# Performance work log

Measured on AMD Instinct MI355X. Metric: run time of the kernel, lower is better.

## Reference

```python
import jax, jax.numpy as jnp
import numpy as np

B, S, D, H = 4, 2048, 1024, 16
HD = D // H  # head_size = 64


def setup_inputs() -> dict:
    key = jax.random.key(0)
    ks = jax.random.split(key, 9)
    sc = 0.02
    x = jax.random.normal(ks[0], (B, S, D), dtype=jnp.float32)
    Wq = jax.random.normal(ks[1], (H, D, HD), dtype=jnp.float32) * sc
    Wk = jax.random.normal(ks[2], (H, D, HD), dtype=jnp.float32) * sc
    Wv = jax.random.normal(ks[3], (H, D, HD), dtype=jnp.float32) * sc
    bq = jax.random.normal(ks[4], (H, HD), dtype=jnp.float32) * sc
    bk = jax.random.normal(ks[5], (H, HD), dtype=jnp.float32) * sc
    bv = jax.random.normal(ks[6], (H, HD), dtype=jnp.float32) * sc
    Wp = jax.random.normal(ks[7], (D, D), dtype=jnp.float32) * sc
    bp = jax.random.normal(ks[8], (D,), dtype=jnp.float32) * sc
    return {"x": x, "Wq": Wq, "bq": bq, "Wk": Wk, "bk": bk,
            "Wv": Wv, "bv": bv, "Wp": Wp, "bp": bp}


def reference(x, Wq, bq, Wk, bk, Wv, bv, Wp, bp):
    # Per-head Linear q/k/v, batched over heads with einsum (equivalent math
    # to the original Python loop over SingleHeadAttention modules).
    q = jnp.einsum('bsd,hde->bhse', x, Wq) + bq[None, :, None, :]
    k = jnp.einsum('bsd,hde->bhse', x, Wk) + bk[None, :, None, :]
    v = jnp.einsum('bsd,hde->bhse', x, Wv) + bv[None, :, None, :]
    att = jnp.einsum('bhqe,bhke->bhqk', q, k) / jnp.sqrt(jnp.asarray(HD, q.dtype))
    causal = jnp.tril(jnp.ones((S, S), dtype=bool))  # [S,S]
    att = jnp.where(causal[None, None], att, jnp.finfo(att.dtype).min)
    w = jax.nn.softmax(att, axis=-1)
    o = jnp.einsum('bhqk,bhke->bhqe', w, v)           # [B,H,S,HD]
    o = o.transpose(0, 2, 1, 3).reshape(B, S, D)      # concat heads on last dim
    # output projection; dropout is identity in eval (p=0.0)
    return jnp.einsum('bsd,de->bse', o, Wp) + bp
```

## Files before the change

kernel.cpp:

```cpp
#include <hip/hip_runtime.h>
#include <hip/hip_bf16.h>

typedef __attribute__((ext_vector_type(8)))  short bf16x8;
typedef __attribute__((ext_vector_type(4)))  float f32x4;
typedef __attribute__((ext_vector_type(16))) float f32x16;
typedef __attribute__((ext_vector_type(2)))  int   i32x2;

#define NH  16
#define HD  64
#define SEQ 2048
#define DM  1024
#define NB  4

#define QSCALE 0.18033688011112042f

#define MFMA(a,b,c)   __builtin_amdgcn_mfma_f32_16x16x32_bf16((a),(b),(c),0,0,0)
#define MFMA32(a,b,c) __builtin_amdgcn_mfma_f32_32x32x16_bf16((a),(b),(c),0,0,0)

static __device__ __forceinline__ void gload_lds16(const void* g, void* l) {
    __builtin_amdgcn_global_load_lds(
        (const __attribute__((address_space(1))) void*)g,
        (__attribute__((address_space(3))) void*)l, 16, 0, 0);
}

__global__ __launch_bounds__(256)
void prep(const float* __restrict__ x,  const float* __restrict__ Wq,
          const float* __restrict__ Wk, const float* __restrict__ Wv,
          const float* __restrict__ Wp,
          __hip_bfloat16* __restrict__ xb,  __hip_bfloat16* __restrict__ wqt,
          __hip_bfloat16* __restrict__ wkt, __hip_bfloat16* __restrict__ wvt,
          __hip_bfloat16* __restrict__ wpt) {
    const long XE = (long)NB * SEQ * DM;
    const long CAST_T = XE / 8;
    long gid = (long)blockIdx.x * 256 + threadIdx.x;
    if (gid < CAST_T) {
        long i = gid * 8;
        float4 a = *reinterpret_cast<const float4*>(x + i);
        float4 b = *reinterpret_cast<const float4*>(x + i + 4);
        ushort4 o1, o2;
        o1.x = __bfloat16_as_ushort(__float2bfloat16(a.x));
        o1.y = __bfloat16_as_ushort(__float2bfloat16(a.y));
        o1.z = __bfloat16_as_ushort(__float2bfloat16(a.z));
        o1.w = __bfloat16_as_ushort(__float2bfloat16(a.w));
        o2.x = __bfloat16_as_ushort(__float2bfloat16(b.x));
        o2.y = __bfloat16_as_ushort(__float2bfloat16(b.y));
        o2.z = __bfloat16_as_ushort(__float2bfloat16(b.z));
        o2.w = __bfloat16_as_ushort(__float2bfloat16(b.w));
        *reinterpret_cast<ushort4*>(xb + i)     = o1;
        *reinterpret_cast<ushort4*>(xb + i + 4) = o2;
        return;
    }
    long r = gid - CAST_T;
    const long WQK = 1 << 20;
    if (r < 3 * WQK) {
        int z = (int)(r >> 20);
        long idx = r & (WQK - 1);
        const float* src = (z == 0) ? Wq : (z == 1) ? Wk : Wv;
        __hip_bfloat16* dst = (z == 0) ? wqt : (z == 1) ? wkt : wvt;
        int c  = (int)(idx & 63);
        long t2 = idx >> 6;
        int rr = (int)(t2 & 1023);
        int mm = (int)(t2 >> 10);
        dst[((long)mm * HD + c) * DM + rr] = __float2bfloat16(src[idx]);
    } else {
        long idx = r - 3 * WQK;
        int c  = (int)(idx & 1023);
        int rr = (int)(idx >> 10);
        wpt[(long)c * DM + rr] = __float2bfloat16(Wp[idx]);
    }
}

__global__ __launch_bounds__(256)
void qkv_gemm(const __hip_bfloat16* __restrict__ A,
              const __hip_bfloat16* __restrict__ BT,
              const float* __restrict__ b0,
              const float* __restrict__ b1,
              const float* __restrict__ b2,
              __hip_bfloat16* __restrict__ Qo,
              __hip_bfloat16* __restrict__ Ko,
              __hip_bfloat16* __restrict__ Vto) {
    __shared__ __align__(16) char lds[2][32768];
    int tid = threadIdx.x;
    int w = tid >> 6, l = tid & 63;
    int lr = l & 15, lg = l >> 4;
    int wr = w >> 1, wc = w & 1;
    int mtile = blockIdx.x, ntile = blockIdx.y;
    const int AR0 = mtile * 128, BR0 = ntile * 128;

    const int rsub = w * 8 + (l >> 3);
    const int sg0 = l & 7;
    auto stage = [&](const __hip_bfloat16* g, int grow0, int kc, char* lbase) {
#pragma unroll
        for (int i = 0; i < 4; ++i) {
            int row = i * 32 + rsub;
            gload_lds16(g + (long)(grow0 + row) * DM + kc + ((sg0 ^ (row & 7)) << 3),
                        lbase + i * 4096 + w * 1024);
        }
    };

    int aoff[4][2], boff[4][2];
#pragma unroll
    for (int m = 0; m < 4; ++m) {
        int ra = wr * 64 + m * 16 + lr;
        int rb = wc * 64 + m * 16 + lr;
#pragma unroll
        for (int kh = 0; kh < 2; ++kh) {
            aoff[m][kh] = ra * 128 + (((kh * 4 + lg) ^ (ra & 7)) << 4);
            boff[m][kh] = 16384 + rb * 128 + (((kh * 4 + lg) ^ (rb & 7)) << 4);
        }
    }

    f32x4 acc[4][4] = {};

    stage(A,  AR0, 0, lds[0]);
    stage(BT, BR0, 0, lds[0] + 16384);
    __syncthreads();

    int cur = 0;
    for (int kt = 0; kt < 16; ++kt) {
        if (kt < 15) {
            int kc = (kt + 1) * 64;
            stage(A,  AR0, kc, lds[cur ^ 1]);
            stage(BT, BR0, kc, lds[cur ^ 1] + 16384);
        }
        bf16x8 bf[4][2];
#pragma unroll
        for (int n = 0; n < 4; ++n) {
            bf[n][0] = *(const bf16x8*)(lds[cur] + boff[n][0]);
            bf[n][1] = *(const bf16x8*)(lds[cur] + boff[n][1]);
        }
#pragma unroll
        for (int m = 0; m < 4; ++m) {
            bf16x8 a0 = *(const bf16x8*)(lds[cur] + aoff[m][0]);
            bf16x8 a1 = *(const bf16x8*)(lds[cur] + aoff[m][1]);
#pragma unroll
            for (int n = 0; n < 4; ++n) {
                acc[m][n] = MFMA(a0, bf[n][0], acc[m][n]);
                acc[m][n] = MFMA(a1, bf[n][1], acc[m][n]);
            }
        }
        __syncthreads();
        cur ^= 1;
    }

    int z = ntile >> 3;
    const float* bias = (z == 0) ? b0 : (z == 1) ? b1 : b2;
    int colbase = (ntile & 7) * 128 + wc * 64;
#pragma unroll
    for (int n = 0; n < 4; ++n) {
        int hc = colbase + n * 16 + lr;
        int h = hc >> 6, e = hc & 63;
        float bb = bias[hc];
#pragma unroll
        for (int m = 0; m < 4; ++m) {
            int row0 = mtile * 128 + wr * 64 + m * 16 + lg * 4;
            int b = row0 >> 11, s0 = row0 & 2047;
            if (z == 0) {
#pragma unroll
                for (int r = 0; r < 4; ++r)
                    Qo[(((long)b * NH + h) * SEQ + s0 + r) * HD + e] =
                        __float2bfloat16((acc[m][n][r] + bb) * QSCALE);
            } else if (z == 1) {
#pragma unroll
                for (int r = 0; r < 4; ++r)
                    Ko[(((long)b * NH + h) * SEQ + s0 + r) * HD + e] =
                        __float2bfloat16(acc[m][n][r] + bb);
            } else {
                ushort4 s4;
                s4.x = __bfloat16_as_ushort(__float2bfloat16(acc[m][n][0] + bb));
                s4.y = __bfloat16_as_ushort(__float2bfloat16(acc[m][n][1] + bb));
                s4.z = __bfloat16_as_ushort(__float2bfloat16(acc[m][n][2] + bb));
                s4.w = __bfloat16_as_ushort(__float2bfloat16(acc[m][n][3] + bb));
                *reinterpret_cast<ushort4*>(
                    Vto + ((long)(b * NH + h) * HD + e) * SEQ + s0) = s4;
            }
        }
    }
}

__global__ __launch_bounds__(256)
void out_gemm(const __hip_bfloat16* __restrict__ A,
              const __hip_bfloat16* __restrict__ BT,
              const float* __restrict__ b0,
              float* __restrict__ Fo) {
    __shared__ __align__(16) char smem[2][16384];
    int tid = threadIdx.x;
    int w = tid >> 6, l = tid & 63;
    int wr = w >> 1, wc = w & 1;
    int lr = l & 15, lg = l >> 4;
    int mtile = blockIdx.x, ntile = blockIdx.y;

    const __hip_bfloat16* Ab = A  + (long)mtile * 128 * DM;
    const __hip_bfloat16* Bb = BT + (long)ntile * 128 * DM;

    const int srow0 = tid >> 2;
    const int srow1 = 64 + srow0;
    const int g0 = (tid & 3) ^ ((srow0 >> 1) & 3);

    int aoff[4], boff[4];
#pragma unroll
    for (int m = 0; m < 4; ++m) {
        int ra = wr * 64 + m * 16 + lr;
        aoff[m] = ra * 64 + ((lg ^ ((ra >> 1) & 3)) * 16);
        int rb = wc * 64 + m * 16 + lr;
        boff[m] = 8192 + rb * 64 + ((lg ^ ((rb >> 1) & 3)) * 16);
    }

    f32x4 acc[4][4] = {};

    {
        char* base = smem[0] + w * 1024;
        gload_lds16(Ab + (long)srow0 * DM + g0 * 8, base);
        gload_lds16(Ab + (long)srow1 * DM + g0 * 8, base + 4096);
        gload_lds16(Bb + (long)srow0 * DM + g0 * 8, base + 8192);
        gload_lds16(Bb + (long)srow1 * DM + g0 * 8, base + 12288);
    }
    __syncthreads();

    int cur = 0;
    for (int kt = 0; kt < 32; ++kt) {
        if (kt != 31) {
            int k0 = (kt + 1) * 32;
            char* base = smem[cur ^ 1] + w * 1024;
            gload_lds16(Ab + (long)srow0 * DM + k0 + g0 * 8, base);
            gload_lds16(Ab + (long)srow1 * DM + k0 + g0 * 8, base + 4096);
            gload_lds16(Bb + (long)srow0 * DM + k0 + g0 * 8, base + 8192);
            gload_lds16(Bb + (long)srow1 * DM + k0 + g0 * 8, base + 12288);
        }
        bf16x8 af[4], bf[4];
#pragma unroll
        for (int m = 0; m < 4; ++m)
            af[m] = *reinterpret_cast<const bf16x8*>(smem[cur] + aoff[m]);
#pragma unroll
        for (int n = 0; n < 4; ++n)
            bf[n] = *reinterpret_cast<const bf16x8*>(smem[cur] + boff[n]);
#pragma unroll
        for (int m = 0; m < 4; ++m)
#pragma unroll
            for (int n = 0; n < 4; ++n)
                acc[m][n] = MFMA(af[m], bf[n], acc[m][n]);
        __syncthreads();
        cur ^= 1;
    }

#pragma unroll
    for (int n = 0; n < 4; ++n) {
        int col = ntile * 128 + wc * 64 + n * 16 + lr;
        float bb = b0[col];
#pragma unroll
        for (int m = 0; m < 4; ++m) {
            long row0 = mtile * 128 + wr * 64 + m * 16 + lg * 4;
#pragma unroll
            for (int r = 0; r < 4; ++r)
                Fo[(row0 + r) * DM + col] = acc[m][n][r] + bb;
        }
    }
}

static __device__ __forceinline__ unsigned pkbf(float a, float b) {
    __hip_bfloat162 h = __float22bfloat162_rn(float2{a, b});
    union { __hip_bfloat162 h2; unsigned u; } u_; u_.h2 = h;
    return u_.u;
}
static __device__ __forceinline__ bf16x8 make_pb(unsigned w0, unsigned w1,
                                                 unsigned w2, unsigned w3) {
    union { unsigned u[4]; bf16x8 v; } u_;
    u_.u[0] = w0; u_.u[1] = w1; u_.u[2] = w2; u_.u[3] = w3;
    return u_.v;
}
static __device__ __forceinline__ i32x2 pl32swap(unsigned a, unsigned b) {
    return __builtin_amdgcn_permlane32_swap((int)a, (int)b, false, false);
}
static __device__ __forceinline__ float xsum32(float x) {
    i32x2 r = pl32swap(__float_as_uint(x), __float_as_uint(x));
    return __uint_as_float((unsigned)r[0]) + __uint_as_float((unsigned)r[1]);
}

template<bool MASKED>
static __device__ __forceinline__ void attn_tile(
    const bf16x8* kf, const bf16x8* qf, const bf16x8* vf,
    int lo5, int hi,
    f32x16& o0, f32x16& o1, float& lsum) {
    f32x16 st = {};
    __builtin_amdgcn_s_setprio(1);
#pragma unroll
    for (int kd = 0; kd < 4; ++kd) st = MFMA32(kf[kd], qf[kd], st);
    __builtin_amdgcn_s_setprio(0);
    if (MASKED) {
#pragma unroll
        for (int r = 0; r < 16; ++r) {
            int kvloc = (r & 3) + 8 * (r >> 2) + 4 * hi;
            st[r] = (kvloc > lo5) ? -INFINITY : st[r];
        }
    }
    float p[16];
#pragma unroll
    for (int r = 0; r < 16; ++r) p[r] = __builtin_amdgcn_exp2f(st[r]);
    float s0 = (p[0] + p[1]) + (p[2] + p[3]);
    float s1 = (p[4] + p[5]) + (p[6] + p[7]);
    float s2 = (p[8] + p[9]) + (p[10] + p[11]);
    float s3 = (p[12] + p[13]) + (p[14] + p[15]);
    lsum += (s0 + s1) + (s2 + s3);

    unsigned pk0 = pkbf(p[0],  p[1]),  pk1 = pkbf(p[2],  p[3]);
    unsigned pk2 = pkbf(p[4],  p[5]),  pk3 = pkbf(p[6],  p[7]);
    unsigned pk4 = pkbf(p[8],  p[9]),  pk5 = pkbf(p[10], p[11]);
    unsigned pk6 = pkbf(p[12], p[13]), pk7 = pkbf(p[14], p[15]);
    i32x2 s02 = pl32swap(pk0, pk2);
    i32x2 s13 = pl32swap(pk1, pk3);
    i32x2 s46 = pl32swap(pk4, pk6);
    i32x2 s57 = pl32swap(pk5, pk7);
    bf16x8 pb0 = make_pb((unsigned)s02[0], (unsigned)s13[0],
                         (unsigned)s02[1], (unsigned)s13[1]);
    bf16x8 pb1 = make_pb((unsigned)s46[0], (unsigned)s57[0],
                         (unsigned)s46[1], (unsigned)s57[1]);

    __builtin_amdgcn_s_setprio(1);
    o0 = MFMA32(vf[0], pb0, o0);
    o1 = MFMA32(vf[1], pb0, o1);
    o0 = MFMA32(vf[2], pb1, o0);
    o1 = MFMA32(vf[3], pb1, o1);
    __builtin_amdgcn_s_setprio(0);
}

__global__ __launch_bounds__(256)
void flash_attn(const __hip_bfloat16* __restrict__ Q,
                const __hip_bfloat16* __restrict__ K,
                const __hip_bfloat16* __restrict__ Vt,
                __hip_bfloat16* __restrict__ O) {
    __shared__ __align__(16) char kv[2][8192];
    int bh = blockIdx.x;
    int w  = threadIdx.x >> 6, l = threadIdx.x & 63;
    int lo5 = l & 31, hi = l >> 5;
    int y  = blockIdx.y;
    int pr = y * 4 + w;
    int jA = pr, jB = 63 - pr;
    int q0A = jA * 32, q0B = jB * 32;
    const int TMAX = 63 - 4 * y;

    const __hip_bfloat16* Qh = Q  + (long)bh * SEQ * HD;
    const __hip_bfloat16* Kh = K  + (long)bh * SEQ * HD;
    const __hip_bfloat16* Vh = Vt + (long)bh * HD * SEQ;

    bf16x8 qfA[4], qfB[4];
#pragma unroll
    for (int kd = 0; kd < 4; ++kd) {
        qfA[kd] = *reinterpret_cast<const bf16x8*>(
            Qh + (long)(q0A + lo5) * HD + kd * 16 + hi * 8);
        qfB[kd] = *reinterpret_cast<const bf16x8*>(
            Qh + (long)(q0B + lo5) * HD + kd * 16 + hi * 8);
    }

    int srow = w * 8 + (l >> 3);
    int kslot = (l & 7) ^ (srow & 7);
    const __hip_bfloat16* ksrc = Kh + (long)srow * HD + kslot * 8;
    int vlog = (l & 7) ^ (srow & 7);
    int vrow = srow + ((vlog >> 2) << 5);
    const __hip_bfloat16* vsrc = Vh + (long)vrow * SEQ + (vlog & 3) * 8;

    int ka[4], va[4];
#pragma unroll
    for (int kd = 0; kd < 4; ++kd)
        ka[kd] = lo5 * 128 + (((kd * 2 + hi) ^ (lo5 & 7)) << 4);
    va[0] = 4096 + lo5 * 128 + (((0 + hi) ^ (lo5 & 7)) << 4);
    va[1] = 4096 + lo5 * 128 + (((4 + hi) ^ (lo5 & 7)) << 4);
    va[2] = 4096 + lo5 * 128 + (((2 + hi) ^ (lo5 & 7)) << 4);
    va[3] = 4096 + lo5 * 128 + (((6 + hi) ^ (lo5 & 7)) << 4);

    f32x16 oA0 = {}, oA1 = {}, oB0 = {}, oB1 = {};
    float lsA = 0.f, lsB = 0.f;

    gload_lds16(ksrc, kv[0] + w * 1024);
    gload_lds16(vsrc, kv[0] + 4096 + w * 1024);
    __syncthreads();

    int buf = 0;
    for (int t = 0; t <= TMAX; ++t) {
        if (t < TMAX) {
            gload_lds16(ksrc + (long)(t + 1) * 32 * HD, kv[buf ^ 1] + w * 1024);
            gload_lds16(vsrc + (t + 1) * 32,            kv[buf ^ 1] + 4096 + w * 1024);
        }
        const char* cb = kv[buf];
        bf16x8 kf[4], vf[4];
#pragma unroll
        for (int kd = 0; kd < 4; ++kd)
            kf[kd] = *reinterpret_cast<const bf16x8*>(cb + ka[kd]);
#pragma unroll
        for (int j = 0; j < 4; ++j)
            vf[j] = *reinterpret_cast<const bf16x8*>(cb + va[j]);

        if (t < jA) {
            attn_tile<false>(kf, qfB, vf, lo5, hi, oB0, oB1, lsB);
            attn_tile<false>(kf, qfA, vf, lo5, hi, oA0, oA1, lsA);
        } else if (t == jA) {
            attn_tile<true >(kf, qfA, vf, lo5, hi, oA0, oA1, lsA);
            attn_tile<false>(kf, qfB, vf, lo5, hi, oB0, oB1, lsB);
        } else if (t < jB) {
            attn_tile<false>(kf, qfB, vf, lo5, hi, oB0, oB1, lsB);
        } else if (t == jB) {
            attn_tile<true >(kf, qfB, vf, lo5, hi, oB0, oB1, lsB);
        }
        __syncthreads();
        buf ^= 1;
    }

    int b = bh >> 4, h = bh & 15;
    float invA = 1.0f / xsum32(lsA);
    float invB = 1.0f / xsum32(lsB);
#pragma unroll
    for (int c = 0; c < 2; ++c) {
        int q0 = c ? q0B : q0A;
        const f32x16& o0 = c ? oB0 : oA0;
        const f32x16& o1 = c ? oB1 : oA1;
        float inv = c ? invB : invA;
        __hip_bfloat16* orow = O + ((long)b * SEQ + q0 + lo5) * DM + h * HD;
#pragma unroll
        for (int nd = 0; nd < 2; ++nd) {
#pragma unroll
            for (int rg = 0; rg < 4; ++rg) {
                ushort4 s4;
                float a0 = (nd ? o1[rg * 4 + 0] : o0[rg * 4 + 0]) * inv;
                float a1 = (nd ? o1[rg * 4 + 1] : o0[rg * 4 + 1]) * inv;
                float a2 = (nd ? o1[rg * 4 + 2] : o0[rg * 4 + 2]) * inv;
                float a3 = (nd ? o1[rg * 4 + 3] : o0[rg * 4 + 3]) * inv;
                s4.x = __bfloat16_as_ushort(__float2bfloat16(a0));
                s4.y = __bfloat16_as_ushort(__float2bfloat16(a1));
                s4.z = __bfloat16_as_ushort(__float2bfloat16(a2));
                s4.w = __bfloat16_as_ushort(__float2bfloat16(a3));
                *reinterpret_cast<ushort4*>(orow + nd * 32 + rg * 8 + hi * 4) = s4;
            }
        }
    }
}

extern "C" void kernel_launch(void* const* d_in, const int* in_sizes, int n_in,
                              void* d_out, int out_size, void* d_ws, size_t ws_size,
                              hipStream_t stream) {
    const float* x  = (const float*)d_in[0];
    const float* Wq = (const float*)d_in[1];
    const float* bq = (const float*)d_in[2];
    const float* Wk = (const float*)d_in[3];
    const float* bk = (const float*)d_in[4];
    const float* Wv = (const float*)d_in[5];
    const float* bv = (const float*)d_in[6];
    const float* Wp = (const float*)d_in[7];
    const float* bp = (const float*)d_in[8];
    float* out = (float*)d_out;

    char* ws = (char*)d_ws;
    const long XE = (long)NB * SEQ * DM;
    const long QKV_ELEMS = (long)NB * NH * SEQ * HD;
    __hip_bfloat16* xb   = (__hip_bfloat16*)ws; ws += XE * 2;
    __hip_bfloat16* Qws  = (__hip_bfloat16*)ws; ws += QKV_ELEMS * 2;
    __hip_bfloat16* Kws  = (__hip_bfloat16*)ws; ws += QKV_ELEMS * 2;
    __hip_bfloat16* Vtws = (__hip_bfloat16*)ws; ws += QKV_ELEMS * 2;
    __hip_bfloat16* Ows  = (__hip_bfloat16*)ws; ws += QKV_ELEMS * 2;
    __hip_bfloat16* wqt  = (__hip_bfloat16*)ws; ws += (long)NH * DM * HD * 2;
    __hip_bfloat16* wkt  = (__hip_bfloat16*)ws; ws += (long)NH * DM * HD * 2;
    __hip_bfloat16* wvt  = (__hip_bfloat16*)ws; ws += (long)NH * DM * HD * 2;
    __hip_bfloat16* wpt  = (__hip_bfloat16*)ws; ws += (long)DM * DM * 2;

    prep<<<20480, 256, 0, stream>>>(x, Wq, Wk, Wv, Wp, xb, wqt, wkt, wvt, wpt);

    qkv_gemm<<<dim3(64, 24), 256, 0, stream>>>(
        xb, wqt, bq, bk, bv, Qws, Kws, Vtws);

    flash_attn<<<dim3(64, 8), 256, 0, stream>>>(Qws, Kws, Vtws, Ows);

    out_gemm<<<dim3(64, 8), 256, 0, stream>>>(Ows, wpt, bp, out);
}
```

Baseline: 185.4 us.

## Use 256x256 tiles with 4-stage pipelined loads for QKV GEMM

The QKV projection GEMM moves from 128x128 tiles with 256 threads and double buffering to 256x256 tiles with 512 threads, a 4-buffer LDS ring with three tiles in flight, explicit vmcnt waits, s_setprio around the MFMA block, and an XCD-aware block swizzle. The out-projection GEMM switches to the 64-wide K-step, 8-way swizzled staging scheme the old QKV kernel used. The aim is more operand reuse per LDS byte, better hiding of global latency and better L2 locality. In exchange it needs 128KB of LDS per block and more accumulator registers, which limits occupancy, and the grid becomes 384 blocks.

```diff
diff --git a/kernel.cpp b/kernel.cpp
--- a/kernel.cpp
+++ b/kernel.cpp
@@ -70,90 +70,100 @@
     }
 }
 
-__global__ __launch_bounds__(256)
-void qkv_gemm(const __hip_bfloat16* __restrict__ A,
-              const __hip_bfloat16* __restrict__ BT,
-              const float* __restrict__ b0,
-              const float* __restrict__ b1,
-              const float* __restrict__ b2,
-              __hip_bfloat16* __restrict__ Qo,
-              __hip_bfloat16* __restrict__ Ko,
-              __hip_bfloat16* __restrict__ Vto) {
-    __shared__ __align__(16) char lds[2][32768];
+__global__ __launch_bounds__(512, 2)
+void qkv_gemm256(const __hip_bfloat16* __restrict__ A,
+                 const __hip_bfloat16* __restrict__ BT,
+                 const float* __restrict__ b0,
+                 const float* __restrict__ b1,
+                 const float* __restrict__ b2,
+                 __hip_bfloat16* __restrict__ Qo,
+                 __hip_bfloat16* __restrict__ Ko,
+                 __hip_bfloat16* __restrict__ Vto) {
+    __shared__ __align__(16) char lds[4][32768];
     int tid = threadIdx.x;
-    int w = tid >> 6, l = tid & 63;
+    int wid = tid >> 6, l = tid & 63;
     int lr = l & 15, lg = l >> 4;
-    int wr = w >> 1, wc = w & 1;
-    int mtile = blockIdx.x, ntile = blockIdx.y;
-    const int AR0 = mtile * 128, BR0 = ntile * 128;
-
-    const int rsub = w * 8 + (l >> 3);
-    const int sg0 = l & 7;
-    auto stage = [&](const __hip_bfloat16* g, int grow0, int kc, char* lbase) {
-#pragma unroll
-        for (int i = 0; i < 4; ++i) {
-            int row = i * 32 + rsub;
-            gload_lds16(g + (long)(grow0 + row) * DM + kc + ((sg0 ^ (row & 7)) << 3),
-                        lbase + i * 4096 + w * 1024);
-        }
-    };
-
-    int aoff[4][2], boff[4][2];
-#pragma unroll
-    for (int m = 0; m < 4; ++m) {
-        int ra = wr * 64 + m * 16 + lr;
-        int rb = wc * 64 + m * 16 + lr;
-#pragma unroll
-        for (int kh = 0; kh < 2; ++kh) {
-            aoff[m][kh] = ra * 128 + (((kh * 4 + lg) ^ (ra & 7)) << 4);
-            boff[m][kh] = 16384 + rb * 128 + (((kh * 4 + lg) ^ (rb & 7)) << 4);
-        }
-    }
-
-    f32x4 acc[4][4] = {};
-
-    stage(A,  AR0, 0, lds[0]);
-    stage(BT, BR0, 0, lds[0] + 16384);
-    __syncthreads();
-
-    int cur = 0;
-    for (int kt = 0; kt < 16; ++kt) {
-        if (kt < 15) {
-            int kc = (kt + 1) * 64;
-            stage(A,  AR0, kc, lds[cur ^ 1]);
-            stage(BT, BR0, kc, lds[cur ^ 1] + 16384);
-        }
-        bf16x8 bf[4][2];
-#pragma unroll
-        for (int n = 0; n < 4; ++n) {
-            bf[n][0] = *(const bf16x8*)(lds[cur] + boff[n][0]);
-            bf[n][1] = *(const bf16x8*)(lds[cur] + boff[n][1]);
-        }
-#pragma unroll
-        for (int m = 0; m < 4; ++m) {
-            bf16x8 a0 = *(const bf16x8*)(lds[cur] + aoff[m][0]);
-            bf16x8 a1 = *(const bf16x8*)(lds[cur] + aoff[m][1]);
-#pragma unroll
-            for (int n = 0; n < 4; ++n) {
-                acc[m][n] = MFMA(a0, bf[n][0], acc[m][n]);
-                acc[m][n] = MFMA(a1, bf[n][1], acc[m][n]);
-            }
-        }
-        __syncthreads();
-        cur ^= 1;
-    }
-
-    int z = ntile >> 3;
+    int wr = wid >> 2, wc = wid & 3;
+
+    int lin = blockIdx.y * 32 + blockIdx.x;
+    int swz = (lin & 7) * 48 + (lin >> 3);
+    int mtile = swz & 31, ntile = swz >> 5;
+    const int  AR0 = mtile * 256;
+    const long BR0 = (long)ntile * 256;
+
+    const int srow = tid >> 2;
+    const int sg   = tid & 3;
+
+    int aoff[8], boff[4];
+#pragma unroll
+    for (int m = 0; m < 8; ++m) {
+        int R = wr * 128 + m * 16 + lr;
+        aoff[m] = R * 64 + (((lg) ^ (R & 3)) << 4);
+    }
+#pragma unroll
+    for (int n = 0; n < 4; ++n) {
+        int R = wc * 64 + n * 16 + lr;
+        boff[n] = 16384 + R * 64 + (((lg) ^ (R & 3)) << 4);
+    }
+
+    f32x4 acc[8][4] = {};
+
+#define STAGE_T(T, BUFI)                                                      \
+    {                                                                         \
+        int kc_ = (T) * 32;                                                   \
+        char* base_ = lds[BUFI];                                              \
+        _Pragma("unroll")                                                     \
+        for (int i_ = 0; i_ < 2; ++i_) {                                      \
+            int row_ = i_ * 128 + srow;                                       \
+            int g_ = sg ^ (row_ & 3);                                         \
+            gload_lds16(A + (long)(AR0 + row_) * DM + kc_ + g_ * 8,           \
+                        base_ + i_ * 8192 + wid * 1024);                      \
+            gload_lds16(BT + (BR0 + row_) * DM + kc_ + g_ * 8,                \
+                        base_ + 16384 + i_ * 8192 + wid * 1024);              \
+        }                                                                     \
+    }
+
+    STAGE_T(0, 0) STAGE_T(1, 1) STAGE_T(2, 2)
+
+#pragma unroll 4
+    for (int t = 0; t < 32; ++t) {
+        const int bufi = t & 3;
+        if (t < 29) STAGE_T(t + 3, (t + 3) & 3)
+        if (t < 29)      { asm volatile("s_waitcnt vmcnt(12)" ::: "memory"); }
+        else if (t == 29){ asm volatile("s_waitcnt vmcnt(8)"  ::: "memory"); }
+        else if (t == 30){ asm volatile("s_waitcnt vmcnt(4)"  ::: "memory"); }
+        else             { asm volatile("s_waitcnt vmcnt(0)"  ::: "memory"); }
+        __builtin_amdgcn_s_barrier();
+        __builtin_amdgcn_sched_barrier(0);
+        const char* cb = lds[bufi];
+        bf16x8 bfr[4];
+#pragma unroll
+        for (int n = 0; n < 4; ++n)
+            bfr[n] = *reinterpret_cast<const bf16x8*>(cb + boff[n]);
+        __builtin_amdgcn_s_setprio(1);
+#pragma unroll
+        for (int m = 0; m < 8; ++m) {
+            bf16x8 a = *reinterpret_cast<const bf16x8*>(cb + aoff[m]);
+#pragma unroll
+            for (int n = 0; n < 4; ++n)
+                acc[m][n] = MFMA(a, bfr[n], acc[m][n]);
+        }
+        __builtin_amdgcn_s_setprio(0);
+        __builtin_amdgcn_s_barrier();
+    }
+#undef STAGE_T
+
+    int z = ntile >> 2;
     const float* bias = (z == 0) ? b0 : (z == 1) ? b1 : b2;
-    int colbase = (ntile & 7) * 128 + wc * 64;
+    int cb0 = (ntile & 3) * 256 + wc * 64;
 #pragma unroll
     for (int n = 0; n < 4; ++n) {
-        int hc = colbase + n * 16 + lr;
+        int hc = cb0 + n * 16 + lr;
         int h = hc >> 6, e = hc & 63;
         float bb = bias[hc];
 #pragma unroll
-        for (int m = 0; m < 4; ++m) {
-            int row0 = mtile * 128 + wr * 64 + m * 16 + lg * 4;
+        for (int m = 0; m < 8; ++m) {
+            int row0 = mtile * 256 + wr * 128 + m * 16 + lg * 4;
             int b = row0 >> 11, s0 = row0 & 2047;
             if (z == 0) {
 #pragma unroll
@@ -183,62 +193,66 @@
               const __hip_bfloat16* __restrict__ BT,
               const float* __restrict__ b0,
               float* __restrict__ Fo) {
-    __shared__ __align__(16) char smem[2][16384];
+    __shared__ __align__(16) char lds[2][32768];
     int tid = threadIdx.x;
     int w = tid >> 6, l = tid & 63;
+    int lr = l & 15, lg = l >> 4;
     int wr = w >> 1, wc = w & 1;
-    int lr = l & 15, lg = l >> 4;
     int mtile = blockIdx.x, ntile = blockIdx.y;
-
-    const __hip_bfloat16* Ab = A  + (long)mtile * 128 * DM;
-    const __hip_bfloat16* Bb = BT + (long)ntile * 128 * DM;
-
-    const int srow0 = tid >> 2;
-    const int srow1 = 64 + srow0;
-    const int g0 = (tid & 3) ^ ((srow0 >> 1) & 3);
-
-    int aoff[4], boff[4];
+    const int AR0 = mtile * 128, BR0 = ntile * 128;
+
+    const int rsub = w * 8 + (l >> 3);
+    const int sg0 = l & 7;
+    auto stage = [&](const __hip_bfloat16* g, int grow0, int kc, char* lbase) {
+#pragma unroll
+        for (int i = 0; i < 4; ++i) {
+            int row = i * 32 + rsub;
+            gload_lds16(g + (long)(grow0 + row) * DM + kc + ((sg0 ^ (row & 7)) << 3),
+                        lbase + i * 4096 + w * 1024);
+        }
+    };
+
+    int aoff[4][2], boff[4][2];
 #pragma unroll
     for (int m = 0; m < 4; ++m) {
         int ra = wr * 64 + m * 16 + lr;
-        aoff[m] = ra * 64 + ((lg ^ ((ra >> 1) & 3)) * 16);
         int rb = wc * 64 + m * 16 + lr;
-        boff[m] = 8192 + rb * 64 + ((lg ^ ((rb >> 1) & 3)) * 16);
+#pragma unroll
+        for (int kh = 0; kh < 2; ++kh) {
+            aoff[m][kh] = ra * 128 + (((kh * 4 + lg) ^ (ra & 7)) << 4);
+            boff[m][kh] = 16384 + rb * 128 + (((kh * 4 + lg) ^ (rb & 7)) << 4);
+        }
     }
 
     f32x4 acc[4][4] = {};
 
-    {
-        char* base = smem[0] + w * 1024;
-        gload_lds16(Ab + (long)srow0 * DM + g0 * 8, base);
-        gload_lds16(Ab + (long)srow1 * DM + g0 * 8, base + 4096);
-        gload_lds16(Bb + (long)srow0 * DM + g0 * 8, base + 8192);
-        gload_lds16(Bb + (long)srow1 * DM + g0 * 8, base + 12288);
-    }
+    stage(A,  AR0, 0, lds[0]);
+    stage(BT, BR0, 0, lds[0] + 16384);
     __syncthreads();
 
     int cur = 0;
-    for (int kt = 0; kt < 32; ++kt) {
-        if (kt != 31) {
-            int k0 = (kt + 1) * 32;
-            char* base = smem[cur ^ 1] + w * 1024;
-            gload_lds16(Ab + (long)srow0 * DM + k0 + g0 * 8, base);
-            gload_lds16(Ab + (long)srow1 * DM + k0 + g0 * 8, base + 4096);
-            gload_lds16(Bb + (long)srow0 * DM + k0 + g0 * 8, base + 8192);
-            gload_lds16(Bb + (long)srow1 * DM + k0 + g0 * 8, base + 12288);
-        }
-        bf16x8 af[4], bf[4];
-#pragma unroll
-        for (int m = 0; m < 4; ++m)
-            af[m] = *reinterpret_cast<const bf16x8*>(smem[cur] + aoff[m]);
-#pragma unroll
-        for (int n = 0; n < 4; ++n)
-            bf[n] = *reinterpret_cast<const bf16x8*>(smem[cur] + boff[n]);
-#pragma unroll
-        for (int m = 0; m < 4; ++m)
-#pragma unroll
-            for (int n = 0; n < 4; ++n)
-                acc[m][n] = MFMA(af[m], bf[n], acc[m][n]);
+    for (int kt = 0; kt < 16; ++kt) {
+        if (kt < 15) {
+            int kc = (kt + 1) * 64;
+            stage(A,  AR0, kc, lds[cur ^ 1]);
+            stage(BT, BR0, kc, lds[cur ^ 1] + 16384);
+        }
+        bf16x8 bf[4][2];
+#pragma unroll
+        for (int n = 0; n < 4; ++n) {
+            bf[n][0] = *(const bf16x8*)(lds[cur] + boff[n][0]);
+            bf[n][1] = *(const bf16x8*)(lds[cur] + boff[n][1]);
+        }
+#pragma unroll
+        for (int m = 0; m < 4; ++m) {
+            bf16x8 a0 = *(const bf16x8*)(lds[cur] + aoff[m][0]);
+            bf16x8 a1 = *(const bf16x8*)(lds[cur] + aoff[m][1]);
+#pragma unroll
+            for (int n = 0; n < 4; ++n) {
+                acc[m][n] = MFMA(a0, bf[n][0], acc[m][n]);
+                acc[m][n] = MFMA(a1, bf[n][1], acc[m][n]);
+            }
+        }
         __syncthreads();
         cur ^= 1;
     }
@@ -462,7 +476,7 @@
 
     prep<<<20480, 256, 0, stream>>>(x, Wq, Wk, Wv, Wp, xb, wqt, wkt, wvt, wpt);
 
-    qkv_gemm<<<dim3(64, 24), 256, 0, stream>>>(
+    qkv_gemm256<<<dim3(32, 12), 512, 0, stream>>>(
         xb, wqt, bq, bk, bv, Qws, Kws, Vtws);
 
     flash_attn<<<dim3(64, 8), 256, 0, stream>>>(Qws, Kws, Vtws, Ows);
```

Result: slower. 197.1 us (+6.3%).
